# Optimization experiments

Measured on AMD Instinct MI355X. Metric: run time of the kernel, lower is better.

Reference implementation:

```python
import jax, jax.numpy as jnp
import numpy as np

N_NODES = 50000
N_EDGES = 800000
N_FEAT, N_HID, N_CLASS = 128, 128, 64


def _sage_conv(x, src, dst, Wl, Wr, b, n_nodes):
    # PyG SAGEConv (mean aggr): out = lin_l(mean_j x_j) + lin_r(x_i)
    msg = x[src]                                            # [E, d] gather
    agg = jax.ops.segment_sum(msg, dst, num_segments=n_nodes)
    deg = jax.ops.segment_sum(jnp.ones_like(dst, dtype=x.dtype), dst,
                              num_segments=n_nodes)
    agg = agg / jnp.maximum(deg, 1.0)[:, None]              # mean over in-neighbors
    return agg @ Wl + x @ Wr + b


def setup_inputs() -> dict:
    key = jax.random.key(0)
    ks = jax.random.split(key, 12)
    x = jax.random.normal(ks[0], (N_NODES, N_FEAT), dtype=jnp.float32)
    edge_index = jax.random.randint(ks[1], (2, N_EDGES), 0, N_NODES, dtype=jnp.int32)

    def glorot(k, fan_in, fan_out):
        s = jnp.sqrt(2.0 / (fan_in + fan_out)).astype(jnp.float32)
        return jax.random.normal(k, (fan_in, fan_out), dtype=jnp.float32) * s

    return {
        "x": x,
        "edge_index": edge_index,
        # layer 0: n_feat -> n_hid
        "Wl0": glorot(ks[2], N_FEAT, N_HID),
        "Wr0": glorot(ks[3], N_FEAT, N_HID),
        "b0": jnp.zeros((N_HID,), dtype=jnp.float32),
        # layer 1 (mid): n_hid -> n_hid
        "Wl1": glorot(ks[4], N_HID, N_HID),
        "Wr1": glorot(ks[5], N_HID, N_HID),
        "b1": jnp.zeros((N_HID,), dtype=jnp.float32),
        # layer 2 (out): n_hid -> n_class
        "Wl2": glorot(ks[6], N_HID, N_CLASS),
        "Wr2": glorot(ks[7], N_HID, N_CLASS),
        "b2": jnp.zeros((N_CLASS,), dtype=jnp.float32),
    }


def reference(x, edge_index, Wl0, Wr0, b0, Wl1, Wr1, b1, Wl2, Wr2, b2):
    src, dst = edge_index[0], edge_index[1]
    n = x.shape[0]
    # in_conv -> relu -> dropout(eval: identity)
    h = jax.nn.relu(_sage_conv(x, src, dst, Wl0, Wr0, b0, n))
    # mid_conv -> relu -> dropout(eval: identity)
    h = jax.nn.relu(_sage_conv(h, src, dst, Wl1, Wr1, b1, n))
    # out_conv (no relu/dropout)
    return _sage_conv(h, src, dst, Wl2, Wr2, b2, n)
```

## Files before the change

### kernel.cpp

```cpp
#include <hip/hip_runtime.h>

#define NFEAT 128
#define RS 128

using bf16x8 = __attribute__((ext_vector_type(8))) short;
using f32x4  = __attribute__((ext_vector_type(4))) float;
using f32x2  = __attribute__((ext_vector_type(2))) float;

__device__ __forceinline__ float bf2f(unsigned short u) {
    union { unsigned int i; float f; } v; v.i = ((unsigned int)u) << 16; return v.f;
}
__device__ __forceinline__ float bfhi2f(unsigned int hi16) {
    union { unsigned int i; float f; } v; v.i = hi16; return v.f;
}
__device__ __forceinline__ unsigned short f2bf(float f) {
    union { float f; unsigned int i; } v; v.f = f;
    unsigned int i = v.i;
    return (unsigned short)((i + 0x7FFFu + ((i >> 16) & 1u)) >> 16);
}
__device__ __forceinline__ unsigned int f4_to_fp8x4(float f0, float f1, float f2, float f3) {
    int p = __builtin_amdgcn_cvt_pk_fp8_f32(f0, f1, 0, false);
    p     = __builtin_amdgcn_cvt_pk_fp8_f32(f2, f3, p, true);
    return (unsigned int)p;
}


__global__ void hist_kernel(const int* __restrict__ dst, int* __restrict__ cnt,
                            int nE, int sliceN) {
    const int slice = blockIdx.x & 7;
    const int lo = slice * sliceN, hi = lo + sliceN;
    const int nb = gridDim.x >> 3;
    const int bs = blockIdx.x >> 3;
    for (int i = bs * 256 + threadIdx.x; i < nE; i += nb * 256) {
        int d = dst[i];
        if (d >= lo && d < hi) atomicAdd(&cnt[d], 1);
    }
}

__global__ void fill_kernel(const int* __restrict__ src, const int* __restrict__ dst,
                            int* __restrict__ cnt, int* __restrict__ col_idx,
                            int nE, int sliceN) {
    const int slice = blockIdx.x & 7;
    const int lo = slice * sliceN, hi = lo + sliceN;
    const int nb = gridDim.x >> 3;
    const int bs = blockIdx.x >> 3;
    for (int i = bs * 256 + threadIdx.x; i < nE; i += nb * 256) {
        int d = dst[i];
        int s = src[i];
        if (d >= lo && d < hi) {
            int pos = atomicAdd(&cnt[d], 1);
            col_idx[pos] = s;
        }
    }
}

__global__ void blocksum_kernel(const int* __restrict__ cnt, int* __restrict__ blockSum, int n) {
    int i = blockIdx.x * 256 + threadIdx.x;
    int d = (i < n) ? cnt[i] : 0;
    int lane = threadIdx.x & 63, wid = threadIdx.x >> 6;
    __shared__ int ws[4];
    int v = d;
    for (int off = 32; off; off >>= 1) v += __shfl_down(v, off);
    if (lane == 0) ws[wid] = v;
    __syncthreads();
    if (threadIdx.x == 0) blockSum[blockIdx.x] = ws[0] + ws[1] + ws[2] + ws[3];
}

__global__ void scan_write_kernel(int* __restrict__ cnt, const int* __restrict__ blockSum,
                                  int* __restrict__ row_ptr, float* __restrict__ inv_deg,
                                  int n) {
    const int b = blockIdx.x, tid = threadIdx.x;
    const int lane = tid & 63, wid = tid >> 6;
    __shared__ int wsA[4];
    __shared__ int wsB[4];
    int v = (tid < b) ? blockSum[tid] : 0;
    for (int off = 32; off; off >>= 1) v += __shfl_down(v, off);
    if (lane == 0) wsA[wid] = v;
    int i = b * 256 + tid;
    int d = (i < n) ? cnt[i] : 0;
    int s = d;
    for (int off = 1; off < 64; off <<= 1) {
        int t = __shfl_up(s, off);
        if (lane >= off) s += t;
    }
    if (lane == 63) wsB[wid] = s;
    __syncthreads();
    int blockOff = wsA[0] + wsA[1] + wsA[2] + wsA[3];
    int wOff = 0;
    for (int w = 0; w < wid; ++w) wOff += wsB[w];
    int excl = blockOff + wOff + s - d;
    if (i < n) {
        row_ptr[i] = excl;
        cnt[i]     = excl;
        inv_deg[i] = 1.0f / (float)(d > 1 ? d : 1);
    }
    if (i == n) row_ptr[n] = excl;
}


__global__ void prep_kernel(const float* __restrict__ x,
                            unsigned short* __restrict__ xc, unsigned char* __restrict__ xq,
                            const float* __restrict__ Wl0, const float* __restrict__ Wr0,
                            const float* __restrict__ Wl1, const float* __restrict__ Wr1,
                            const float* __restrict__ Wl2, const float* __restrict__ Wr2,
                            unsigned short* __restrict__ Wsz0,
                            unsigned short* __restrict__ Wsz1,
                            unsigned short* __restrict__ Wsz2,
                            int* __restrict__ cnt, int n) {
    int idx = blockIdx.x * 256 + threadIdx.x;
    const int R0 = n * 32;
    if (idx < R0) {
        int node = idx >> 5, fb = (idx & 31) * 4;
        float4 v = *(const float4*)(x + (size_t)node * NFEAT + fb);
        uint2 hw;
        hw.x = (unsigned int)f2bf(v.x) | ((unsigned int)f2bf(v.y) << 16);
        hw.y = (unsigned int)f2bf(v.z) | ((unsigned int)f2bf(v.w) << 16);
        *(uint2*)(xc + (size_t)node * RS + fb) = hw;
        *(unsigned int*)(xq + (size_t)node * NFEAT + fb) = f4_to_fp8x4(v.x, v.y, v.z, v.w);
        return;
    }
    idx -= R0;
    if (idx < 81920) {
        const float* Wl; const float* Wr; unsigned short* Wsz; int nout; int li;
        if (idx < 32768)      { Wl = Wl0; Wr = Wr0; Wsz = Wsz0; nout = 128; li = idx; }
        else if (idx < 65536) { Wl = Wl1; Wr = Wr1; Wsz = Wsz1; nout = 128; li = idx - 32768; }
        else                  { Wl = Wl2; Wr = Wr2; Wsz = Wsz2; nout = 64;  li = idx - 65536; }
        int c = li >> 8, k = li & 255;
        float f = (k < 128) ? Wl[k * nout + c] : Wr[(k - 128) * nout + c];
        Wsz[c * 256 + (k ^ ((c & 7) << 3))] = f2bf(f);
        return;
    }
    idx -= 81920;
    if (idx < n) cnt[idx] = 0;
}


template<int NOUT, bool RELU, bool FINAL>
__global__ __launch_bounds__(512, 4) void layer_kernel(
    const unsigned char* __restrict__ xq, const unsigned short* __restrict__ xc,
    const int* __restrict__ row_ptr, const int* __restrict__ col_idx,
    const float* __restrict__ inv_deg,
    const unsigned short* __restrict__ Wsz, const float* __restrict__ bias,
    float* __restrict__ outF, unsigned short* __restrict__ outC,
    unsigned char* __restrict__ outQ, int n)
{
    constexpr int HALVES = NOUT / 64;
    constexpr int AOFF = 32768;
    __shared__ char smem[32768 + 16384];
    const int tid  = threadIdx.x;
    const int lane = tid & 63;
    const int wid  = tid >> 6;
    const int rowBase = blockIdx.x * 64;

    {
        const char* wsrc = (const char*)Wsz;
        #pragma unroll
        for (int i = 0; i < 4; ++i) {
            const int off = (i * 512 + tid) * 16;
            __builtin_amdgcn_global_load_lds(
                (const __attribute__((address_space(1))) unsigned int*)(wsrc + off),
                (__attribute__((address_space(3))) unsigned int*)(smem + off),
                16, 0, 0);
        }
    }

    const int lrow = lane & 15;
    const int lk   = (lane >> 4) * 8;
    const int rg   = wid >> 1;
    const int cg   = wid & 1;
    int r0 = rowBase + rg * 16 + lrow; if (r0 > n - 1) r0 = n - 1;
    const unsigned short* Xr = xc + (size_t)r0 * RS;
    bf16x8 xr[4];
    #pragma unroll
    for (int ks = 0; ks < 4; ++ks) xr[ks] = *(const bf16x8*)(Xr + ks * 32 + lk);
    __builtin_amdgcn_sched_barrier(0);

    {
        const int l    = tid & 7;
        const int nd   = tid >> 3;
        const int node = rowBase + nd;
        if (node < n) {
            int beg = row_ptr[node], end = row_ptr[node + 1];
            float a[2][16];
            #pragma unroll
            for (int u = 0; u < 2; ++u)
                #pragma unroll
                for (int j = 0; j < 16; ++j) a[u][j] = 0.f;
            auto acc16 = [&](float* A, uint4 v) {
                f32x2 d;
                d = __builtin_amdgcn_cvt_pk_f32_fp8(v.x, false); A[0]  += d[0]; A[1]  += d[1];
                d = __builtin_amdgcn_cvt_pk_f32_fp8(v.x, true);  A[2]  += d[0]; A[3]  += d[1];
                d = __builtin_amdgcn_cvt_pk_f32_fp8(v.y, false); A[4]  += d[0]; A[5]  += d[1];
                d = __builtin_amdgcn_cvt_pk_f32_fp8(v.y, true);  A[6]  += d[0]; A[7]  += d[1];
                d = __builtin_amdgcn_cvt_pk_f32_fp8(v.z, false); A[8]  += d[0]; A[9]  += d[1];
                d = __builtin_amdgcn_cvt_pk_f32_fp8(v.z, true);  A[10] += d[0]; A[11] += d[1];
                d = __builtin_amdgcn_cvt_pk_f32_fp8(v.w, false); A[12] += d[0]; A[13] += d[1];
                d = __builtin_amdgcn_cvt_pk_f32_fp8(v.w, true);  A[14] += d[0]; A[15] += d[1];
            };
            int e = beg;
            for (; e + 8 <= end; e += 8) {
                uint4 v[8];
                #pragma unroll
                for (int u = 0; u < 8; ++u) {
                    int s = col_idx[e + u];
                    v[u] = *(const uint4*)(xq + (size_t)s * NFEAT + l * 16);
                }
                #pragma unroll
                for (int u = 0; u < 8; ++u) acc16(a[u & 1], v[u]);
            }
            for (; e < end; ++e) {
                int s = col_idx[e];
                uint4 v = *(const uint4*)(xq + (size_t)s * NFEAT + l * 16);
                acc16(a[0], v);
            }
            float sc = inv_deg[node];
            unsigned short hs[16];
            #pragma unroll
            for (int j = 0; j < 16; ++j)
                hs[j] = f2bf((a[0][j] + a[1][j]) * sc);
            uint4 h0, h1;
            h0.x = (unsigned int)hs[0]  | ((unsigned int)hs[1]  << 16);
            h0.y = (unsigned int)hs[2]  | ((unsigned int)hs[3]  << 16);
            h0.z = (unsigned int)hs[4]  | ((unsigned int)hs[5]  << 16);
            h0.w = (unsigned int)hs[6]  | ((unsigned int)hs[7]  << 16);
            h1.x = (unsigned int)hs[8]  | ((unsigned int)hs[9]  << 16);
            h1.y = (unsigned int)hs[10] | ((unsigned int)hs[11] << 16);
            h1.z = (unsigned int)hs[12] | ((unsigned int)hs[13] << 16);
            h1.w = (unsigned int)hs[14] | ((unsigned int)hs[15] << 16);
            const int s_ = nd & 7;
            char* arow = smem + AOFF + nd * 256;
            *(uint4*)(arow + (((2 * l)     ^ s_) << 4)) = h0;
            *(uint4*)(arow + (((2 * l + 1) ^ s_) << 4)) = h1;
        }
    }

    __syncthreads();

    const int cc0 = cg * 32 + lrow;
    const int cc1 = cg * 32 + 16 + lrow;
    const int cb0 = (cc0 << 9) + ((lane >> 4) * 16), xm0 = (cc0 & 7) << 4;
    const int cb1 = (cc1 << 9) + ((lane >> 4) * 16), xm1 = (cc1 & 7) << 4;
    const int ar    = rg * 16 + lrow;
    const int abase = AOFF + ar * 256;
    const int as    = ar & 7;

    #pragma unroll
    for (int h = 0; h < HALVES; ++h) {
        if (h > 0) {
            __syncthreads();
            const char* wsrc = (const char*)(Wsz + (size_t)h * 64 * 256);
            #pragma unroll
            for (int i = 0; i < 4; ++i) {
                const int off = (i * 512 + tid) * 16;
                __builtin_amdgcn_global_load_lds(
                    (const __attribute__((address_space(1))) unsigned int*)(wsrc + off),
                    (__attribute__((address_space(3))) unsigned int*)(smem + off),
                    16, 0, 0);
            }
            __syncthreads();
        }

        f32x4 acc0 = (f32x4){0.f, 0.f, 0.f, 0.f};
        f32x4 acc1 = (f32x4){0.f, 0.f, 0.f, 0.f};

        #pragma unroll
        for (int ks = 0; ks < 8; ++ks) {
            bf16x8 a;
            if (ks < 4)
                a = *(const bf16x8*)(smem + abase + (((ks * 4 + (lane >> 4)) ^ as) << 4));
            else
                a = xr[ks - 4];
            bf16x8 b0 = *(const bf16x8*)(smem + ((cb0 + (ks << 6)) ^ xm0));
            bf16x8 b1 = *(const bf16x8*)(smem + ((cb1 + (ks << 6)) ^ xm1));
            acc0 = __builtin_amdgcn_mfma_f32_16x16x32_bf16(a, b0, acc0, 0, 0, 0);
            acc1 = __builtin_amdgcn_mfma_f32_16x16x32_bf16(a, b1, acc1, 0, 0, 0);
        }

        #pragma unroll
        for (int nf = 0; nf < 2; ++nf) {
            const f32x4 av = nf ? acc1 : acc0;
            const int c = h * 64 + cg * 32 + nf * 16 + lrow;
            const float bv = bias[c];
            #pragma unroll
            for (int reg = 0; reg < 4; ++reg) {
                const int r = rowBase + rg * 16 + (lane >> 4) * 4 + reg;
                if (r < n) {
                    float hv = av[reg] + bv;
                    if (RELU) hv = fmaxf(hv, 0.f);
                    if (FINAL) {
                        outF[(size_t)r * NOUT + c] = hv;
                    } else {
                        outC[(size_t)r * RS + c] = f2bf(hv);
                        outQ[(size_t)r * NFEAT + c] =
                            (unsigned char)(__builtin_amdgcn_cvt_pk_fp8_f32(hv, hv, 0, false) & 0xFF);
                    }
                }
            }
        }
    }
}

extern "C" void kernel_launch(void* const* d_in, const int* in_sizes, int n_in,
                              void* d_out, int out_size, void* d_ws, size_t ws_size,
                              hipStream_t stream) {
    const float* x   = (const float*)d_in[0];
    const int*   ei  = (const int*)d_in[1];
    const float* Wl0 = (const float*)d_in[2];
    const float* Wr0 = (const float*)d_in[3];
    const float* b0  = (const float*)d_in[4];
    const float* Wl1 = (const float*)d_in[5];
    const float* Wr1 = (const float*)d_in[6];
    const float* b1  = (const float*)d_in[7];
    const float* Wl2 = (const float*)d_in[8];
    const float* Wr2 = (const float*)d_in[9];
    const float* b2  = (const float*)d_in[10];

    const int nN = in_sizes[0] / NFEAT;
    const int nE = in_sizes[1] / 2;
    const int* src = ei;
    const int* dst = ei + nE;

    char* ws = (char*)d_ws;
    size_t off = 0;
    auto take = [&](size_t bytes) { char* p = ws + off; off += (bytes + 255) & ~(size_t)255; return p; };
    int*   cnt      = (int*)  take((size_t)nN * 4);
    int*   row_ptr  = (int*)  take((size_t)(nN + 1) * 4);
    int*   col_idx  = (int*)  take((size_t)nE * 4);
    float* inv_deg  = (float*)take((size_t)nN * 4);
    int*   blockSum = (int*)  take(256 * 4);
    const size_t plane  = (size_t)nN * RS * 2;
    const size_t qplane = (size_t)nN * NFEAT;
    unsigned short* xc0  = (unsigned short*)take(plane);
    unsigned short* xc1  = (unsigned short*)take(plane);
    unsigned char*  xq0  = (unsigned char*) take(qplane);
    unsigned char*  xq1  = (unsigned char*) take(qplane);
    unsigned short* Wsz0 = (unsigned short*)take(128 * 256 * 2);
    unsigned short* Wsz1 = (unsigned short*)take(128 * 256 * 2);
    unsigned short* Wsz2 = (unsigned short*)take(64 * 256 * 2);
    (void)ws_size; (void)n_in; (void)out_size;

    const int scanBlocks = (nN + 255) / 256;
    const int sliceN = (nN + 7) / 8;

    const int prepTotal = nN * 32 + 81920 + nN;
    prep_kernel<<<(prepTotal + 255) / 256, 256, 0, stream>>>(
        x, xc0, xq0, Wl0, Wr0, Wl1, Wr1, Wl2, Wr2, Wsz0, Wsz1, Wsz2, cnt, nN);

    hist_kernel<<<2048, 256, 0, stream>>>(dst, cnt, nE, sliceN);
    blocksum_kernel<<<scanBlocks, 256, 0, stream>>>(cnt, blockSum, nN);
    scan_write_kernel<<<scanBlocks, 256, 0, stream>>>(cnt, blockSum, row_ptr, inv_deg, nN);
    fill_kernel<<<2048, 256, 0, stream>>>(src, dst, cnt, col_idx, nE, sliceN);

    const int layerGrid = (nN + 63) / 64;

    layer_kernel<128, true, false><<<layerGrid, 512, 0, stream>>>(
        xq0, xc0, row_ptr, col_idx, inv_deg, Wsz0, b0, nullptr, xc1, xq1, nN);
    layer_kernel<128, true, false><<<layerGrid, 512, 0, stream>>>(
        xq1, xc1, row_ptr, col_idx, inv_deg, Wsz1, b1, nullptr, xc0, xq0, nN);
    layer_kernel<64, false, true><<<layerGrid, 512, 0, stream>>>(
        xq0, xc0, row_ptr, col_idx, inv_deg, Wsz2, b2, (float*)d_out, nullptr, nullptr, nN);
}
```

Before: 205.6 us.

## Sort nodes by in-degree via counting-sort permutation to balance layer gather work

Adds a degree histogram, a bin scan and a scatter kernel that build a permutation of nodes grouped by in-degree. Each layer kernel then processes rows in permuted order, so lanes within a wavefront walk neighbor lists of similar length and diverge less in the gather loop. Outputs are written back through the permutation. The cost is two extra small kernel launches plus histogram atomics, one extra indirection per row, and scattered (non-contiguous) row loads and output stores, which can hurt memory coalescing.

```diff
diff --git a/kernel.cpp b/kernel.cpp
--- a/kernel.cpp
+++ b/kernel.cpp
@@ -9,9 +9,6 @@
 
 __device__ __forceinline__ float bf2f(unsigned short u) {
     union { unsigned int i; float f; } v; v.i = ((unsigned int)u) << 16; return v.f;
-}
-__device__ __forceinline__ float bfhi2f(unsigned int hi16) {
-    union { unsigned int i; float f; } v; v.i = hi16; return v.f;
 }
 __device__ __forceinline__ unsigned short f2bf(float f) {
     union { float f; unsigned int i; } v; v.f = f;
@@ -68,7 +65,7 @@
 
 __global__ void scan_write_kernel(int* __restrict__ cnt, const int* __restrict__ blockSum,
                                   int* __restrict__ row_ptr, float* __restrict__ inv_deg,
-                                  int n) {
+                                  int* __restrict__ degHist, int n) {
     const int b = blockIdx.x, tid = threadIdx.x;
     const int lane = tid & 63, wid = tid >> 6;
     __shared__ int wsA[4];
@@ -93,8 +90,36 @@
         row_ptr[i] = excl;
         cnt[i]     = excl;
         inv_deg[i] = 1.0f / (float)(d > 1 ? d : 1);
+        atomicAdd(&degHist[d > 255 ? 255 : d], 1);
     }
     if (i == n) row_ptr[n] = excl;
+}
+
+__global__ void bin_scan_kernel(int* __restrict__ dh) {
+    const int tid = threadIdx.x, lane = tid & 63, w = tid >> 6;
+    __shared__ int ws[4];
+    int v = dh[tid];
+    int s = v;
+    for (int off = 1; off < 64; off <<= 1) {
+        int t = __shfl_up(s, off);
+        if (lane >= off) s += t;
+    }
+    if (lane == 63) ws[w] = s;
+    __syncthreads();
+    int woff = 0;
+    for (int i = 0; i < w; ++i) woff += ws[i];
+    dh[tid] = woff + s - v;
+}
+
+__global__ void scatter_kernel(const int* __restrict__ row_ptr, int* __restrict__ cursor,
+                               int* __restrict__ perm, int n) {
+    int i = blockIdx.x * 256 + threadIdx.x;
+    if (i < n) {
+        int d = row_ptr[i + 1] - row_ptr[i];
+        if (d > 255) d = 255;
+        int pos = atomicAdd(&cursor[d], 1);
+        perm[pos] = i;
+    }
 }
 
 
@@ -106,7 +131,7 @@
                             unsigned short* __restrict__ Wsz0,
                             unsigned short* __restrict__ Wsz1,
                             unsigned short* __restrict__ Wsz2,
-                            int* __restrict__ cnt, int n) {
+                            int* __restrict__ cnt, int* __restrict__ degHist, int n) {
     int idx = blockIdx.x * 256 + threadIdx.x;
     const int R0 = n * 32;
     if (idx < R0) {
@@ -131,7 +156,9 @@
         return;
     }
     idx -= 81920;
-    if (idx < n) cnt[idx] = 0;
+    if (idx < n) { cnt[idx] = 0; return; }
+    idx -= n;
+    if (idx < 256) degHist[idx] = 0;
 }
 
 
@@ -139,7 +166,7 @@
 __global__ __launch_bounds__(512, 4) void layer_kernel(
     const unsigned char* __restrict__ xq, const unsigned short* __restrict__ xc,
     const int* __restrict__ row_ptr, const int* __restrict__ col_idx,
-    const float* __restrict__ inv_deg,
+    const float* __restrict__ inv_deg, const int* __restrict__ perm,
     const unsigned short* __restrict__ Wsz, const float* __restrict__ bias,
     float* __restrict__ outF, unsigned short* __restrict__ outC,
     unsigned char* __restrict__ outQ, int n)
@@ -168,8 +195,9 @@
     const int lk   = (lane >> 4) * 8;
     const int rg   = wid >> 1;
     const int cg   = wid & 1;
-    int r0 = rowBase + rg * 16 + lrow; if (r0 > n - 1) r0 = n - 1;
-    const unsigned short* Xr = xc + (size_t)r0 * RS;
+    int ri0 = rowBase + rg * 16 + lrow; if (ri0 > n - 1) ri0 = n - 1;
+    const int xnode = perm[ri0];
+    const unsigned short* Xr = xc + (size_t)xnode * RS;
     bf16x8 xr[4];
     #pragma unroll
     for (int ks = 0; ks < 4; ++ks) xr[ks] = *(const bf16x8*)(Xr + ks * 32 + lk);
@@ -178,60 +206,59 @@
     {
         const int l    = tid & 7;
         const int nd   = tid >> 3;
-        const int node = rowBase + nd;
-        if (node < n) {
-            int beg = row_ptr[node], end = row_ptr[node + 1];
-            float a[2][16];
-            #pragma unroll
-            for (int u = 0; u < 2; ++u)
-                #pragma unroll
-                for (int j = 0; j < 16; ++j) a[u][j] = 0.f;
-            auto acc16 = [&](float* A, uint4 v) {
-                f32x2 d;
-                d = __builtin_amdgcn_cvt_pk_f32_fp8(v.x, false); A[0]  += d[0]; A[1]  += d[1];
-                d = __builtin_amdgcn_cvt_pk_f32_fp8(v.x, true);  A[2]  += d[0]; A[3]  += d[1];
-                d = __builtin_amdgcn_cvt_pk_f32_fp8(v.y, false); A[4]  += d[0]; A[5]  += d[1];
-                d = __builtin_amdgcn_cvt_pk_f32_fp8(v.y, true);  A[6]  += d[0]; A[7]  += d[1];
-                d = __builtin_amdgcn_cvt_pk_f32_fp8(v.z, false); A[8]  += d[0]; A[9]  += d[1];
-                d = __builtin_amdgcn_cvt_pk_f32_fp8(v.z, true);  A[10] += d[0]; A[11] += d[1];
-                d = __builtin_amdgcn_cvt_pk_f32_fp8(v.w, false); A[12] += d[0]; A[13] += d[1];
-                d = __builtin_amdgcn_cvt_pk_f32_fp8(v.w, true);  A[14] += d[0]; A[15] += d[1];
-            };
-            int e = beg;
-            for (; e + 8 <= end; e += 8) {
-                uint4 v[8];
-                #pragma unroll
-                for (int u = 0; u < 8; ++u) {
-                    int s = col_idx[e + u];
-                    v[u] = *(const uint4*)(xq + (size_t)s * NFEAT + l * 16);
-                }
-                #pragma unroll
-                for (int u = 0; u < 8; ++u) acc16(a[u & 1], v[u]);
+        int pidx = rowBase + nd; if (pidx > n - 1) pidx = n - 1;
+        const int node = perm[pidx];
+        int beg = row_ptr[node], end = row_ptr[node + 1];
+        float a[2][16];
+        #pragma unroll
+        for (int u = 0; u < 2; ++u)
+            #pragma unroll
+            for (int j = 0; j < 16; ++j) a[u][j] = 0.f;
+        auto acc16 = [&](float* A, uint4 v) {
+            f32x2 d;
+            d = __builtin_amdgcn_cvt_pk_f32_fp8(v.x, false); A[0]  += d[0]; A[1]  += d[1];
+            d = __builtin_amdgcn_cvt_pk_f32_fp8(v.x, true);  A[2]  += d[0]; A[3]  += d[1];
+            d = __builtin_amdgcn_cvt_pk_f32_fp8(v.y, false); A[4]  += d[0]; A[5]  += d[1];
+            d = __builtin_amdgcn_cvt_pk_f32_fp8(v.y, true);  A[6]  += d[0]; A[7]  += d[1];
+            d = __builtin_amdgcn_cvt_pk_f32_fp8(v.z, false); A[8]  += d[0]; A[9]  += d[1];
+            d = __builtin_amdgcn_cvt_pk_f32_fp8(v.z, true);  A[10] += d[0]; A[11] += d[1];
+            d = __builtin_amdgcn_cvt_pk_f32_fp8(v.w, false); A[12] += d[0]; A[13] += d[1];
+            d = __builtin_amdgcn_cvt_pk_f32_fp8(v.w, true);  A[14] += d[0]; A[15] += d[1];
+        };
+        int e = beg;
+        for (; e + 8 <= end; e += 8) {
+            uint4 v[8];
+            #pragma unroll
+            for (int u = 0; u < 8; ++u) {
+                int s = col_idx[e + u];
+                v[u] = *(const uint4*)(xq + (size_t)s * NFEAT + l * 16);
             }
-            for (; e < end; ++e) {
-                int s = col_idx[e];
-                uint4 v = *(const uint4*)(xq + (size_t)s * NFEAT + l * 16);
-                acc16(a[0], v);
-            }
-            float sc = inv_deg[node];
-            unsigned short hs[16];
-            #pragma unroll
-            for (int j = 0; j < 16; ++j)
-                hs[j] = f2bf((a[0][j] + a[1][j]) * sc);
-            uint4 h0, h1;
-            h0.x = (unsigned int)hs[0]  | ((unsigned int)hs[1]  << 16);
-            h0.y = (unsigned int)hs[2]  | ((unsigned int)hs[3]  << 16);
-            h0.z = (unsigned int)hs[4]  | ((unsigned int)hs[5]  << 16);
-            h0.w = (unsigned int)hs[6]  | ((unsigned int)hs[7]  << 16);
-            h1.x = (unsigned int)hs[8]  | ((unsigned int)hs[9]  << 16);
-            h1.y = (unsigned int)hs[10] | ((unsigned int)hs[11] << 16);
-            h1.z = (unsigned int)hs[12] | ((unsigned int)hs[13] << 16);
-            h1.w = (unsigned int)hs[14] | ((unsigned int)hs[15] << 16);
-            const int s_ = nd & 7;
-            char* arow = smem + AOFF + nd * 256;
-            *(uint4*)(arow + (((2 * l)     ^ s_) << 4)) = h0;
-            *(uint4*)(arow + (((2 * l + 1) ^ s_) << 4)) = h1;
-        }
+            #pragma unroll
+            for (int u = 0; u < 8; ++u) acc16(a[u & 1], v[u]);
+        }
+        for (; e < end; ++e) {
+            int s = col_idx[e];
+            uint4 v = *(const uint4*)(xq + (size_t)s * NFEAT + l * 16);
+            acc16(a[0], v);
+        }
+        float sc = inv_deg[node];
+        unsigned short hs[16];
+        #pragma unroll
+        for (int j = 0; j < 16; ++j)
+            hs[j] = f2bf((a[0][j] + a[1][j]) * sc);
+        uint4 h0, h1;
+        h0.x = (unsigned int)hs[0]  | ((unsigned int)hs[1]  << 16);
+        h0.y = (unsigned int)hs[2]  | ((unsigned int)hs[3]  << 16);
+        h0.z = (unsigned int)hs[4]  | ((unsigned int)hs[5]  << 16);
+        h0.w = (unsigned int)hs[6]  | ((unsigned int)hs[7]  << 16);
+        h1.x = (unsigned int)hs[8]  | ((unsigned int)hs[9]  << 16);
+        h1.y = (unsigned int)hs[10] | ((unsigned int)hs[11] << 16);
+        h1.z = (unsigned int)hs[12] | ((unsigned int)hs[13] << 16);
+        h1.w = (unsigned int)hs[14] | ((unsigned int)hs[15] << 16);
+        const int s_ = nd & 7;
+        char* arow = smem + AOFF + nd * 256;
+        *(uint4*)(arow + (((2 * l)     ^ s_) << 4)) = h0;
+        *(uint4*)(arow + (((2 * l + 1) ^ s_) << 4)) = h1;
     }
 
     __syncthreads();
@@ -243,6 +270,14 @@
     const int ar    = rg * 16 + lrow;
     const int abase = AOFF + ar * 256;
     const int as    = ar & 7;
+
+    int rout[4];
+    #pragma unroll
+    for (int reg = 0; reg < 4; ++reg) {
+        int ri = rowBase + rg * 16 + (lane >> 4) * 4 + reg;
+        if (ri > n - 1) ri = n - 1;
+        rout[reg] = perm[ri];
+    }
 
     #pragma unroll
     for (int h = 0; h < HALVES; ++h) {
@@ -283,17 +318,15 @@
             const float bv = bias[c];
             #pragma unroll
             for (int reg = 0; reg < 4; ++reg) {
-                const int r = rowBase + rg * 16 + (lane >> 4) * 4 + reg;
-                if (r < n) {
-                    float hv = av[reg] + bv;
-                    if (RELU) hv = fmaxf(hv, 0.f);
-                    if (FINAL) {
-                        outF[(size_t)r * NOUT + c] = hv;
-                    } else {
-                        outC[(size_t)r * RS + c] = f2bf(hv);
-                        outQ[(size_t)r * NFEAT + c] =
-                            (unsigned char)(__builtin_amdgcn_cvt_pk_fp8_f32(hv, hv, 0, false) & 0xFF);
-                    }
+                const int r = rout[reg];
+                float hv = av[reg] + bv;
+                if (RELU) hv = fmaxf(hv, 0.f);
+                if (FINAL) {
+                    outF[(size_t)r * NOUT + c] = hv;
+                } else {
+                    outC[(size_t)r * RS + c] = f2bf(hv);
+                    outQ[(size_t)r * NFEAT + c] =
+                        (unsigned char)(__builtin_amdgcn_cvt_pk_fp8_f32(hv, hv, 0, false) & 0xFF);
                 }
             }
         }
@@ -328,6 +361,8 @@
     int*   col_idx  = (int*)  take((size_t)nE * 4);
     float* inv_deg  = (float*)take((size_t)nN * 4);
     int*   blockSum = (int*)  take(256 * 4);
+    int*   degHist  = (int*)  take(256 * 4);
+    int*   perm     = (int*)  take((size_t)nN * 4);
     const size_t plane  = (size_t)nN * RS * 2;
     const size_t qplane = (size_t)nN * NFEAT;
     unsigned short* xc0  = (unsigned short*)take(plane);
@@ -342,21 +377,23 @@
     const int scanBlocks = (nN + 255) / 256;
     const int sliceN = (nN + 7) / 8;
 
-    const int prepTotal = nN * 32 + 81920 + nN;
+    const int prepTotal = nN * 32 + 81920 + nN + 256;
     prep_kernel<<<(prepTotal + 255) / 256, 256, 0, stream>>>(
-        x, xc0, xq0, Wl0, Wr0, Wl1, Wr1, Wl2, Wr2, Wsz0, Wsz1, Wsz2, cnt, nN);
+        x, xc0, xq0, Wl0, Wr0, Wl1, Wr1, Wl2, Wr2, Wsz0, Wsz1, Wsz2, cnt, degHist, nN);
 
     hist_kernel<<<2048, 256, 0, stream>>>(dst, cnt, nE, sliceN);
     blocksum_kernel<<<scanBlocks, 256, 0, stream>>>(cnt, blockSum, nN);
-    scan_write_kernel<<<scanBlocks, 256, 0, stream>>>(cnt, blockSum, row_ptr, inv_deg, nN);
+    scan_write_kernel<<<scanBlocks, 256, 0, stream>>>(cnt, blockSum, row_ptr, inv_deg, degHist, nN);
     fill_kernel<<<2048, 256, 0, stream>>>(src, dst, cnt, col_idx, nE, sliceN);
+    bin_scan_kernel<<<1, 256, 0, stream>>>(degHist);
+    scatter_kernel<<<scanBlocks, 256, 0, stream>>>(row_ptr, degHist, perm, nN);
 
     const int layerGrid = (nN + 63) / 64;
 
     layer_kernel<128, true, false><<<layerGrid, 512, 0, stream>>>(
-        xq0, xc0, row_ptr, col_idx, inv_deg, Wsz0, b0, nullptr, xc1, xq1, nN);
+        xq0, xc0, row_ptr, col_idx, inv_deg, perm, Wsz0, b0, nullptr, xc1, xq1, nN);
     layer_kernel<128, true, false><<<layerGrid, 512, 0, stream>>>(
-        xq1, xc1, row_ptr, col_idx, inv_deg, Wsz1, b1, nullptr, xc0, xq0, nN);
+        xq1, xc1, row_ptr, col_idx, inv_deg, perm, Wsz1, b1, nullptr, xc0, xq0, nN);
     layer_kernel<64, false, true><<<layerGrid, 512, 0, stream>>>(
-        xq0, xc0, row_ptr, col_idx, inv_deg, Wsz2, b2, (float*)d_out, nullptr, nullptr, nN);
-}
+        xq0, xc0, row_ptr, col_idx, inv_deg, perm, Wsz2, b2, (float*)d_out, nullptr, nullptr, nN);
+}
```

New measurement: 460.7 us. +124.1%, slower.
